# Kernel optimization log

Hardware: AMD Instinct MI355X
Metric: run time of the kernel (lower is better)

Reference implementation:

```python
import jax, jax.numpy as jnp
import numpy as np

DIM = 256
H_GLOBAL = 8
H_LOCAL = 4  # max(1, num_heads // 2)
WINDOW = 5
HALF = WINDOW // 2
B, S = 4, 2048
EPS = 1e-5


def layer_norm(x, g, b):
    mu = jnp.mean(x, axis=-1, keepdims=True)
    var = jnp.mean(jnp.square(x - mu), axis=-1, keepdims=True)
    return (x - mu) * jax.lax.rsqrt(var + EPS) * g + b


def qkv_proj(x, in_w, in_b):
    qkv = x @ in_w.T + in_b
    return jnp.split(qkv, 3, axis=-1)


def global_mha(x, in_w, in_b, out_w, out_b, nh):
    Bq, Sq, D = x.shape
    hd = D // nh
    q, k, v = qkv_proj(x, in_w, in_b)
    q = q.reshape(Bq, Sq, nh, hd)
    k = k.reshape(Bq, Sq, nh, hd)
    v = v.reshape(Bq, Sq, nh, hd)
    scores = jnp.einsum('bqhd,bkhd->bhqk', q, k) / np.sqrt(hd).astype(np.float32)
    attn = jax.nn.softmax(scores, axis=-1)
    o = jnp.einsum('bhqk,bkhd->bqhd', attn, v).reshape(Bq, Sq, D)
    return o @ out_w.T + out_b


def local_mha(x, in_w, in_b, out_w, out_b, nh):
    # banded sliding-window attention, window = 2*HALF+1, per-query softmax
    Bq, Sq, D = x.shape
    hd = D // nh
    q, k, v = qkv_proj(x, in_w, in_b)
    kp = jnp.pad(k, ((0, 0), (HALF, HALF), (0, 0)))
    vp = jnp.pad(v, ((0, 0), (HALF, HALF), (0, 0)))
    # [B, S, W, D] windows of keys/values around each query position
    k_win = jnp.stack([kp[:, j:j + Sq] for j in range(WINDOW)], axis=2)
    v_win = jnp.stack([vp[:, j:j + Sq] for j in range(WINDOW)], axis=2)
    q = q.reshape(Bq, Sq, nh, hd)
    k_win = k_win.reshape(Bq, Sq, WINDOW, nh, hd)
    v_win = v_win.reshape(Bq, Sq, WINDOW, nh, hd)
    scores = jnp.einsum('bshd,bswhd->bshw', q, k_win) / np.sqrt(hd).astype(np.float32)
    idx = jnp.arange(Sq)[:, None] + jnp.arange(-HALF, HALF + 1)[None, :]  # [S, W]
    valid = (idx >= 0) & (idx < Sq)
    scores = jnp.where(valid[None, :, None, :], scores, -jnp.inf)
    attn = jax.nn.softmax(scores, axis=-1)
    o = jnp.einsum('bshw,bswhd->bshd', attn, v_win).reshape(Bq, Sq, D)
    return o @ out_w.T + out_b


def setup_inputs() -> dict:
    key = jax.random.key(0)
    ks = jax.random.split(key, 8)
    sc = 0.02
    d = DIM
    return {
        'x': jax.random.normal(ks[0], (B, S, d), jnp.float32),
        'g_in_w': jax.random.normal(ks[1], (3 * d, d), jnp.float32) * sc,
        'g_in_b': jnp.zeros((3 * d,), jnp.float32),
        'g_out_w': jax.random.normal(ks[2], (d, d), jnp.float32) * sc,
        'g_out_b': jnp.zeros((d,), jnp.float32),
        't_in_w': jax.random.normal(ks[3], (3 * d, d), jnp.float32) * sc,
        't_in_b': jnp.zeros((3 * d,), jnp.float32),
        't_out_w': jax.random.normal(ks[4], (d, d), jnp.float32) * sc,
        't_out_b': jnp.zeros((d,), jnp.float32),
        'fus_w1': jax.random.normal(ks[5], (2 * d, 2 * d), jnp.float32) * sc,
        'fus_b1': jnp.zeros((2 * d,), jnp.float32),
        'fus_w2': jax.random.normal(ks[6], (d, 2 * d), jnp.float32) * sc,
        'fus_b2': jnp.zeros((d,), jnp.float32),
        'ffn_w1': jax.random.normal(ks[7], (2 * d, d), jnp.float32) * sc,
        'ffn_b1': jnp.zeros((2 * d,), jnp.float32),
        'ffn_w2': jax.random.normal(jax.random.fold_in(key, 9), (d, 2 * d), jnp.float32) * sc,
        'ffn_b2': jnp.zeros((d,), jnp.float32),
        'gn_g': jnp.ones((d,), jnp.float32),
        'gn_b': jnp.zeros((d,), jnp.float32),
        'fn_g': jnp.ones((d,), jnp.float32),
        'fn_b': jnp.zeros((d,), jnp.float32),
    }


def reference(x, g_in_w, g_in_b, g_out_w, g_out_b,
              t_in_w, t_in_b, t_out_w, t_out_b,
              fus_w1, fus_b1, fus_w2, fus_b2,
              ffn_w1, ffn_b1, ffn_w2, ffn_b2,
              gn_g, gn_b, fn_g, fn_b):
    x_global = global_mha(x, g_in_w, g_in_b, g_out_w, g_out_b, H_GLOBAL)
    x_local = local_mha(x, t_in_w, t_in_b, t_out_w, t_out_b, H_LOCAL)
    x_comb = jnp.concatenate([x_global, x_local], axis=-1)
    x_fused = jax.nn.silu(x_comb @ fus_w1.T + fus_b1) @ fus_w2.T + fus_b2
    x = layer_norm(x + x_fused, gn_g, gn_b)
    x_ffn = jax.nn.silu(x @ ffn_w1.T + ffn_b1) @ ffn_w2.T + ffn_b2
    x = layer_norm(x + x_ffn, fn_g, fn_b)
    return x
```

## Files before the change

### kernel.cpp

```cpp
#include <hip/hip_runtime.h>

constexpr int Bb = 4;
constexpr int Ss = 2048;
constexpr int QSTR = 1536;

typedef __bf16 bf16x8 __attribute__((ext_vector_type(8)));
typedef __bf16 bf16x4 __attribute__((ext_vector_type(4)));
typedef float  f32x4  __attribute__((ext_vector_type(4)));
typedef unsigned int uint2v __attribute__((ext_vector_type(2)));
typedef unsigned int uint4v __attribute__((ext_vector_type(4)));

__device__ __forceinline__ void glds16(const void* g, void* l) {
    __builtin_amdgcn_global_load_lds(
        (const __attribute__((address_space(1))) unsigned int*)g,
        (__attribute__((address_space(3))) unsigned int*)l, 16, 0, 0);
}

__device__ __forceinline__ void xpose4(unsigned int& a, unsigned int& b) {
    uint2v r = __builtin_amdgcn_permlane32_swap(a, b, false, false);
    uint2v u = __builtin_amdgcn_permlane16_swap(r[0], r[1], false, false);
    a = u[0]; b = u[1];
}

__device__ __forceinline__ unsigned int exp2_pk(float a, float b) {
    float ea = __builtin_amdgcn_exp2f(a);
    float eb = __builtin_amdgcn_exp2f(b);
    unsigned int r;
    asm("v_cvt_pk_bf16_f32 %0, %1, %2" : "=v"(r) : "v"(ea), "v"(eb));
    return r;
}

struct CvtArgs {
    const float* src[9];
    __bf16* dst[9];
    int start[10];
};

__global__ __launch_bounds__(256) void convert_all(CvtArgs a)
{
    int e = 0;
    const int bid = blockIdx.x;
#pragma unroll
    for (int i = 0; i < 8; i++) if (bid >= a.start[i + 1]) e = i + 1;
    const int idx = (bid - a.start[e]) * 256 + threadIdx.x;
    const float* s = a.src[e];
    float4 v0 = *(const float4*)&s[(size_t)idx * 8];
    float4 v1 = *(const float4*)&s[(size_t)idx * 8 + 4];
    bf16x8 o;
    o[0] = (__bf16)v0.x; o[1] = (__bf16)v0.y; o[2] = (__bf16)v0.z; o[3] = (__bf16)v0.w;
    o[4] = (__bf16)v1.x; o[5] = (__bf16)v1.y; o[6] = (__bf16)v1.z; o[7] = (__bf16)v1.w;
    *(bf16x8*)&a.dst[e][(size_t)idx * 8] = o;
}

__global__ __launch_bounds__(256) void gemm128(
    const __bf16* __restrict__ A, const __bf16* __restrict__ W,
    const float* __restrict__ bias, const float* __restrict__ bias2, int bsplit,
    __bf16* __restrict__ C, int K, int ldc)
{
    __shared__ __bf16 As[128 * 64];
    __shared__ __bf16 Ws[128 * 64];
    const int tid = threadIdx.x;
    const int lane = tid & 63;
    const int wv = tid >> 6;
    const int wm = (wv >> 1) * 64;
    const int wn = (wv & 1) * 64;
    const int qrow = lane & 15;
    const int quad = lane >> 4;
    const int n0 = blockIdx.x * 128;
    const int m0 = blockIdx.y * 128;

    f32x4 acc[4][4];
#pragma unroll
    for (int i = 0; i < 4; i++)
#pragma unroll
        for (int j = 0; j < 4; j++) acc[i][j] = {0.f, 0.f, 0.f, 0.f};

    for (int k0 = 0; k0 < K; k0 += 64) {
        __syncthreads();
#pragma unroll
        for (int i = 0; i < 4; i++) {
            const int c = (wv * 4 + i) * 64 + lane;
            const int row = c >> 3, g = c & 7;
            const int gs = (g ^ (row & 7)) * 8;
            glds16(&A[(size_t)(m0 + row) * K + k0 + gs], &As[(wv * 4 + i) * 512]);
            glds16(&W[(size_t)(n0 + row) * K + k0 + gs], &Ws[(wv * 4 + i) * 512]);
        }
        __syncthreads();
#pragma unroll
        for (int ksub = 0; ksub < 2; ksub++) {
            const int gl = ksub * 4 + quad;
            bf16x8 af[4], bf[4];
#pragma unroll
            for (int mi = 0; mi < 4; mi++) {
                const int row = wm + mi * 16 + qrow;
                af[mi] = *(const bf16x8*)&As[row * 64 + (gl ^ (row & 7)) * 8];
            }
#pragma unroll
            for (int ni = 0; ni < 4; ni++) {
                const int row = wn + ni * 16 + qrow;
                bf[ni] = *(const bf16x8*)&Ws[row * 64 + (gl ^ (row & 7)) * 8];
            }
#pragma unroll
            for (int mi = 0; mi < 4; mi++)
#pragma unroll
                for (int ni = 0; ni < 4; ni++)
                    acc[mi][ni] = __builtin_amdgcn_mfma_f32_16x16x32_bf16(
                        af[mi], bf[ni], acc[mi][ni], 0, 0, 0);
        }
    }

    float bz[4];
#pragma unroll
    for (int ni = 0; ni < 4; ni++) {
        const int n = n0 + wn + ni * 16 + qrow;
        bz[ni] = (n < bsplit) ? bias[n] : bias2[n - bsplit];
    }
#pragma unroll
    for (int mi = 0; mi < 4; mi++)
#pragma unroll
        for (int r = 0; r < 4; r++) {
            const int row = m0 + wm + mi * 16 + quad * 4 + r;
#pragma unroll
            for (int ni = 0; ni < 4; ni++) {
                float v = acc[mi][ni][r] + bz[ni];
                C[(size_t)row * ldc + n0 + wn + ni * 16 + qrow] = (__bf16)v;
            }
        }
}

template<bool SILU, bool OUT_BF16>
__global__ __launch_bounds__(256) void gemm_mid(
    const __bf16* __restrict__ A0, const __bf16* __restrict__ W0,
    const float* __restrict__ bias0, const __bf16* __restrict__ W1,
    const float* __restrict__ bias1, int nsplit, int aoff1, int coff1,
    void* __restrict__ C, int lda, int K, int ldc)
{
    __shared__ __bf16 As[64 * 128];
    __shared__ __bf16 Ws[64 * 128];
    const int tid = threadIdx.x;
    const int lane = tid & 63;
    const int wv = tid >> 6;
    const int wm = (wv >> 1) * 32;
    const int wn = (wv & 1) * 32;
    const int qrow = lane & 15;
    const int quad = lane >> 4;
    const bool second = (int)blockIdx.x >= nsplit;
    const int bx = second ? (blockIdx.x - nsplit) : blockIdx.x;
    const __bf16* A = second ? (A0 + aoff1) : A0;
    const __bf16* W = second ? W1 : W0;
    const float* bias = second ? bias1 : bias0;
    const int coff = second ? coff1 : 0;
    const int n0 = bx * 64;
    const int m0 = blockIdx.y * 64;

    f32x4 acc[2][2];
#pragma unroll
    for (int i = 0; i < 2; i++)
#pragma unroll
        for (int j = 0; j < 2; j++) acc[i][j] = {0.f, 0.f, 0.f, 0.f};

    for (int k0 = 0; k0 < K; k0 += 128) {
        __syncthreads();
#pragma unroll
        for (int i = 0; i < 4; i++) {
            const int c = (wv * 4 + i) * 64 + lane;
            const int row = c >> 4, s = c & 15;
            const int gs = ((s & 8) | ((s ^ row) & 7)) * 8;
            glds16(&A[(size_t)(m0 + row) * lda + k0 + gs], &As[(wv * 4 + i) * 512]);
            glds16(&W[(size_t)(n0 + row) * K + k0 + gs], &Ws[(wv * 4 + i) * 512]);
        }
        __syncthreads();
#pragma unroll
        for (int ksub = 0; ksub < 4; ksub++) {
            const int gl = ksub * 4 + quad;
            bf16x8 af[2], bf[2];
#pragma unroll
            for (int mi = 0; mi < 2; mi++) {
                const int row = wm + mi * 16 + qrow;
                const int s = (gl & 8) | ((gl ^ row) & 7);
                af[mi] = *(const bf16x8*)&As[row * 128 + s * 8];
            }
#pragma unroll
            for (int ni = 0; ni < 2; ni++) {
                const int row = wn + ni * 16 + qrow;
                const int s = (gl & 8) | ((gl ^ row) & 7);
                bf[ni] = *(const bf16x8*)&Ws[row * 128 + s * 8];
            }
#pragma unroll
            for (int mi = 0; mi < 2; mi++)
#pragma unroll
                for (int ni = 0; ni < 2; ni++)
                    acc[mi][ni] = __builtin_amdgcn_mfma_f32_16x16x32_bf16(
                        af[mi], bf[ni], acc[mi][ni], 0, 0, 0);
        }
    }

    float bz[2];
#pragma unroll
    for (int ni = 0; ni < 2; ni++) bz[ni] = bias[n0 + wn + ni * 16 + qrow];

#pragma unroll
    for (int mi = 0; mi < 2; mi++)
#pragma unroll
        for (int r = 0; r < 4; r++) {
            const int row = m0 + wm + mi * 16 + quad * 4 + r;
#pragma unroll
            for (int ni = 0; ni < 2; ni++) {
                float v = acc[mi][ni][r] + bz[ni];
                if (SILU) v = v / (1.f + __expf(-v));
                const int col = coff + n0 + wn + ni * 16 + qrow;
                if (OUT_BF16)
                    ((__bf16*)C)[(size_t)row * ldc + col] = (__bf16)v;
                else
                    ((float*)C)[(size_t)row * ldc + col] = v;
            }
        }
}

template<bool OBF>
__global__ __launch_bounds__(256) void gemm_ln(
    const __bf16* __restrict__ A, const __bf16* __restrict__ W,
    const float* __restrict__ bias, const float* __restrict__ res,
    const float* __restrict__ g, const float* __restrict__ be,
    float* __restrict__ out, __bf16* __restrict__ outb)
{
    __shared__ __bf16 As[16 * 128];
    __shared__ __bf16 Ws[256 * 128];
    __shared__ float lnp[2][16][4];
    const int tid = threadIdx.x;
    const int lane = tid & 63;
    const int wv = tid >> 6;
    const int qrow = lane & 15;
    const int quad = lane >> 4;
    const int m0 = blockIdx.x * 16;

    f32x4 acc[4];
#pragma unroll
    for (int ni = 0; ni < 4; ni++) acc[ni] = {0.f, 0.f, 0.f, 0.f};

    for (int k0 = 0; k0 < 512; k0 += 128) {
        __syncthreads();
        {
            const int c = wv * 64 + lane;
            const int row = c >> 4, s = c & 15;
            const int gs = ((s & 8) | ((s ^ row) & 7)) * 8;
            glds16(&A[(size_t)(m0 + row) * 512 + k0 + gs], &As[wv * 512]);
        }
#pragma unroll
        for (int i = 0; i < 16; i++) {
            const int c = (wv * 16 + i) * 64 + lane;
            const int row = c >> 4, s = c & 15;
            const int gs = ((s & 8) | ((s ^ row) & 7)) * 8;
            glds16(&W[(size_t)row * 512 + k0 + gs], &Ws[(wv * 16 + i) * 512]);
        }
        __syncthreads();
#pragma unroll
        for (int ksub = 0; ksub < 4; ksub++) {
            const int gl = ksub * 4 + quad;
            bf16x8 af, bf[4];
            {
                const int row = qrow;
                const int s = (gl & 8) | ((gl ^ row) & 7);
                af = *(const bf16x8*)&As[row * 128 + s * 8];
            }
#pragma unroll
            for (int ni = 0; ni < 4; ni++) {
                const int row = wv * 64 + ni * 16 + qrow;
                const int s = (gl & 8) | ((gl ^ row) & 7);
                bf[ni] = *(const bf16x8*)&Ws[row * 128 + s * 8];
            }
#pragma unroll
            for (int ni = 0; ni < 4; ni++)
                acc[ni] = __builtin_amdgcn_mfma_f32_16x16x32_bf16(
                    af, bf[ni], acc[ni], 0, 0, 0);
        }
    }

    f32x4 d[4];
#pragma unroll
    for (int ni = 0; ni < 4; ni++) {
        const int f = wv * 64 + ni * 16 + qrow;
        const float bz = bias[f];
#pragma unroll
        for (int r = 0; r < 4; r++)
            d[ni][r] = acc[ni][r] + bz + res[(size_t)(m0 + quad * 4 + r) * 256 + f];
    }

    f32x4 ps;
#pragma unroll
    for (int r = 0; r < 4; r++) ps[r] = d[0][r] + d[1][r] + d[2][r] + d[3][r];
#pragma unroll
    for (int off = 1; off <= 8; off <<= 1)
#pragma unroll
        for (int r = 0; r < 4; r++) ps[r] += __shfl_xor(ps[r], off, 64);
    if (qrow == 0)
#pragma unroll
        for (int r = 0; r < 4; r++) lnp[0][quad * 4 + r][wv] = ps[r];
    __syncthreads();
    float mu[4];
#pragma unroll
    for (int r = 0; r < 4; r++) {
        const int t = quad * 4 + r;
        mu[r] = (lnp[0][t][0] + lnp[0][t][1] + lnp[0][t][2] + lnp[0][t][3]) * (1.f / 256.f);
    }

#pragma unroll
    for (int r = 0; r < 4; r++) {
        float a0 = d[0][r] - mu[r], a1 = d[1][r] - mu[r];
        float a2 = d[2][r] - mu[r], a3 = d[3][r] - mu[r];
        ps[r] = a0 * a0 + a1 * a1 + a2 * a2 + a3 * a3;
    }
#pragma unroll
    for (int off = 1; off <= 8; off <<= 1)
#pragma unroll
        for (int r = 0; r < 4; r++) ps[r] += __shfl_xor(ps[r], off, 64);
    if (qrow == 0)
#pragma unroll
        for (int r = 0; r < 4; r++) lnp[1][quad * 4 + r][wv] = ps[r];
    __syncthreads();
    float rsv[4];
#pragma unroll
    for (int r = 0; r < 4; r++) {
        const int t = quad * 4 + r;
        float v = (lnp[1][t][0] + lnp[1][t][1] + lnp[1][t][2] + lnp[1][t][3]) * (1.f / 256.f);
        rsv[r] = rsqrtf(v + 1e-5f);
    }

#pragma unroll
    for (int ni = 0; ni < 4; ni++) {
        const int f = wv * 64 + ni * 16 + qrow;
        const float gg = g[f];
        const float bb = be[f];
#pragma unroll
        for (int r = 0; r < 4; r++) {
            const size_t idx = (size_t)(m0 + quad * 4 + r) * 256 + f;
            float o = (d[ni][r] - mu[r]) * rsv[r] * gg + bb;
            out[idx] = o;
            if (OBF) outb[idx] = (__bf16)o;
        }
    }
}

__global__ __launch_bounds__(512) void attn_fused(
    const __bf16* __restrict__ qkv, __bf16* __restrict__ Op,
    float* __restrict__ Lp, __bf16* __restrict__ acat)
{
    __shared__ __bf16 Kl[2][64 * 32];
    __shared__ __bf16 Vt[2][32 * 72];

    const int t = threadIdx.x;
    const int lane = t & 63;
    const int wv = t >> 6;

    if (blockIdx.x < 1024) {
        const int bid = blockIdx.x;
        const int sp = bid & 3;
        const int qc = (bid >> 2) & 7;
        const int h  = (bid >> 5) & 7;
        const int b  = bid >> 8;
        const int bS = b * Ss;
        const int q0 = qc * 256;

        const int qrow = lane & 15;
        const int quad = lane >> 4;
        const float cQ = 1.4426950408889634f * 0.17677669529663687f;

        bf16x8 qf[2];
#pragma unroll
        for (int tl = 0; tl < 2; tl++) {
            bf16x8 qraw = *(const bf16x8*)(qkv +
                (size_t)(bS + q0 + wv * 32 + tl * 16 + qrow) * QSTR + h * 32 + quad * 8);
#pragma unroll
            for (int i = 0; i < 8; i++) qf[tl][i] = (__bf16)((float)qraw[i] * cQ);
        }
        bf16x8 ones;
#pragma unroll
        for (int i = 0; i < 8; i++) ones[i] = (__bf16)1.0f;

        f32x4 o0[2], o1[2], lac[2];
#pragma unroll
        for (int tl = 0; tl < 2; tl++) {
            o0[tl] = {0.f, 0.f, 0.f, 0.f};
            o1[tl] = {0.f, 0.f, 0.f, 0.f};
            lac[tl] = {0.f, 0.f, 0.f, 0.f};
        }
        const f32x4 z = {0.f, 0.f, 0.f, 0.f};

        const int kc_c = wv * 64 + lane;
        const int kkey = kc_c >> 2, kdg = kc_c & 3;
        const int vkey = t & 63, vq = t >> 6;
        const int kc0 = sp * 8;

        bf16x4 vreg = *(const bf16x4*)(qkv +
            (size_t)(bS + kc0 * 64 + vkey) * QSTR + 512 + h * 32 + vq * 4);
        if (wv < 4)
            glds16(qkv + (size_t)(bS + kc0 * 64 + kkey) * QSTR + 256 + h * 32 + kdg * 8,
                   &Kl[0][wv * 512]);

        for (int i = 0; i < 8; i++) {
            const int cur = i & 1;
#pragma unroll
            for (int e = 0; e < 4; e++) Vt[cur][(vq * 4 + e) * 72 + vkey] = vreg[e];
            __syncthreads();
            const int nx = (i < 7) ? (kc0 + i + 1) : (kc0 + 7);
            vreg = *(const bf16x4*)(qkv +
                (size_t)(bS + nx * 64 + vkey) * QSTR + 512 + h * 32 + vq * 4);
            if (i < 7 && wv < 4)
                glds16(qkv + (size_t)(bS + nx * 64 + kkey) * QSTR + 256 + h * 32 + kdg * 8,
                       &Kl[1 - cur][wv * 512]);

            bf16x8 kf[4];
#pragma unroll
            for (int kg = 0; kg < 4; kg++)
                kf[kg] = *(const bf16x8*)&Kl[cur][(kg * 16 + qrow) * 32 + quad * 8];
            bf16x8 vf00 = *(const bf16x8*)&Vt[cur][qrow * 72 + quad * 8];
            bf16x8 vf01 = *(const bf16x8*)&Vt[cur][qrow * 72 + 32 + quad * 8];
            bf16x8 vf10 = *(const bf16x8*)&Vt[cur][(16 + qrow) * 72 + quad * 8];
            bf16x8 vf11 = *(const bf16x8*)&Vt[cur][(16 + qrow) * 72 + 32 + quad * 8];

#pragma unroll
            for (int tl = 0; tl < 2; tl++) {
                f32x4 s[4];
#pragma unroll
                for (int kg = 0; kg < 4; kg++)
                    s[kg] = __builtin_amdgcn_mfma_f32_16x16x32_bf16(
                        kf[kg], qf[tl], z, 0, 0, 0);
                unsigned int R[4][2];
#pragma unroll
                for (int kg = 0; kg < 4; kg++) {
                    R[kg][0] = exp2_pk(s[kg][0], s[kg][1]);
                    R[kg][1] = exp2_pk(s[kg][2], s[kg][3]);
                }
                xpose4(R[0][0], R[1][0]);
                xpose4(R[0][1], R[1][1]);
                xpose4(R[2][0], R[3][0]);
                xpose4(R[2][1], R[3][1]);
                uint4v p0u = {R[0][0], R[0][1], R[1][0], R[1][1]};
                uint4v p1u = {R[2][0], R[2][1], R[3][0], R[3][1]};
                bf16x8 pf0 = __builtin_bit_cast(bf16x8, p0u);
                bf16x8 pf1 = __builtin_bit_cast(bf16x8, p1u);

                o0[tl] = __builtin_amdgcn_mfma_f32_16x16x32_bf16(vf00, pf0, o0[tl], 0, 0, 0);
                o1[tl] = __builtin_amdgcn_mfma_f32_16x16x32_bf16(vf10, pf0, o1[tl], 0, 0, 0);
                lac[tl] = __builtin_amdgcn_mfma_f32_16x16x32_bf16(ones, pf0, lac[tl], 0, 0, 0);
                o0[tl] = __builtin_amdgcn_mfma_f32_16x16x32_bf16(vf01, pf1, o0[tl], 0, 0, 0);
                o1[tl] = __builtin_amdgcn_mfma_f32_16x16x32_bf16(vf11, pf1, o1[tl], 0, 0, 0);
                lac[tl] = __builtin_amdgcn_mfma_f32_16x16x32_bf16(ones, pf1, lac[tl], 0, 0, 0);
            }
        }

#pragma unroll
        for (int tl = 0; tl < 2; tl++) {
            const int gid = (b * 8 + h) * 2048 + q0 + wv * 32 + tl * 16 + qrow;
            __bf16* po = Op + (size_t)sp * 2097152 + (size_t)gid * 32;
            bf16x4 w0, w1;
#pragma unroll
            for (int r = 0; r < 4; r++) {
                w0[r] = (__bf16)o0[tl][r];
                w1[r] = (__bf16)o1[tl][r];
            }
            *(bf16x4*)&po[quad * 4]      = w0;
            *(bf16x4*)&po[16 + quad * 4] = w1;
            if (quad == 0) Lp[sp * 65536 + gid] = lac[tl][0];
        }
    } else {
        const int w = (blockIdx.x - 1024) * 8 + wv;
        const int g = lane >> 3;
        const int l8 = lane & 7;
        const int R = w * 8 + g;
        const int h = R & 3;
        const int s = (R >> 2) & 2047;
        const int b = R >> 13;

        float qv[8];
        {
            bf16x8 q8 = *(const bf16x8*)&qkv[(size_t)(b * Ss + s) * QSTR + 768 + h * 64 + l8 * 8];
#pragma unroll
            for (int e = 0; e < 8; e++) qv[e] = (float)q8[e];
        }

        float sc[5];
        bf16x8 v8[5];
#pragma unroll
        for (int j = 0; j < 5; j++) {
            int pos = s + j - 2;
            bool valid = (pos >= 0) && (pos < Ss);
            int cpos = valid ? pos : 0;
            const size_t rb = (size_t)(b * Ss + cpos) * QSTR;
            bf16x8 k8 = *(const bf16x8*)&qkv[rb + 1024 + h * 64 + l8 * 8];
            v8[j]     = *(const bf16x8*)&qkv[rb + 1280 + h * 64 + l8 * 8];
            float p = 0.f;
#pragma unroll
            for (int e = 0; e < 8; e++) p += qv[e] * (float)k8[e];
            p += __shfl_xor(p, 1, 64);
            p += __shfl_xor(p, 2, 64);
            p += __shfl_xor(p, 4, 64);
            sc[j] = valid ? p * 0.125f : -1e30f;
        }
        float m = sc[0];
#pragma unroll
        for (int j = 1; j < 5; j++) m = fmaxf(m, sc[j]);
        float l = 0.f;
        float o[8];
#pragma unroll
        for (int e = 0; e < 8; e++) o[e] = 0.f;
#pragma unroll
        for (int j = 0; j < 5; j++) {
            float pe = __builtin_amdgcn_exp2f((sc[j] - m) * 1.4426950408889634f);
            l += pe;
#pragma unroll
            for (int e = 0; e < 8; e++) o[e] += pe * (float)v8[j][e];
        }
        const float li = 1.f / l;
        bf16x8 r;
#pragma unroll
        for (int e = 0; e < 8; e++) r[e] = (__bf16)(o[e] * li);
        *(bf16x8*)&acat[(size_t)(b * Ss + s) * 512 + 256 + h * 64 + l8 * 8] = r;
    }
}

__global__ __launch_bounds__(256) void attn_combine(
    const __bf16* __restrict__ Op, const float* __restrict__ Lp,
    __bf16* __restrict__ acat)
{
    const int t = blockIdx.x * 256 + threadIdx.x;
    const int gid = t >> 3;
    const int dg = t & 7;
    const int b = gid >> 14;
    const int h = (gid >> 11) & 7;
    const int q = gid & 2047;

    const float li = 1.f / (Lp[gid] + Lp[65536 + gid] +
                            Lp[131072 + gid] + Lp[196608 + gid]);
    const __bf16* base = Op + (size_t)gid * 32 + dg * 4;
    bf16x4 a0 = *(const bf16x4*)&base[0];
    bf16x4 a1 = *(const bf16x4*)&base[2097152];
    bf16x4 a2 = *(const bf16x4*)&base[4194304];
    bf16x4 a3 = *(const bf16x4*)&base[6291456];
    bf16x4 r;
#pragma unroll
    for (int i = 0; i < 4; i++)
        r[i] = (__bf16)(((float)a0[i] + (float)a1[i] +
                         (float)a2[i] + (float)a3[i]) * li);
    *(bf16x4*)&acat[(size_t)(b * Ss + q) * 512 + h * 32 + dg * 4] = r;
}

extern "C" void kernel_launch(void* const* d_in, const int* in_sizes, int n_in,
                              void* d_out, int out_size, void* d_ws, size_t ws_size,
                              hipStream_t stream)
{
    const float* x      = (const float*)d_in[0];
    const float* g_in_w = (const float*)d_in[1];
    const float* g_in_b = (const float*)d_in[2];
    const float* g_out_w= (const float*)d_in[3];
    const float* g_out_b= (const float*)d_in[4];
    const float* t_in_w = (const float*)d_in[5];
    const float* t_in_b = (const float*)d_in[6];
    const float* t_out_w= (const float*)d_in[7];
    const float* t_out_b= (const float*)d_in[8];
    const float* fus_w1 = (const float*)d_in[9];
    const float* fus_b1 = (const float*)d_in[10];
    const float* fus_w2 = (const float*)d_in[11];
    const float* fus_b2 = (const float*)d_in[12];
    const float* ffn_w1 = (const float*)d_in[13];
    const float* ffn_b1 = (const float*)d_in[14];
    const float* ffn_w2 = (const float*)d_in[15];
    const float* ffn_b2 = (const float*)d_in[16];
    const float* gn_g   = (const float*)d_in[17];
    const float* gn_b   = (const float*)d_in[18];
    const float* fn_g   = (const float*)d_in[19];
    const float* fn_b   = (const float*)d_in[20];
    float* out = (float*)d_out;
    float* ws  = (float*)d_ws;

    __bf16* xb     = (__bf16*)(ws);
    __bf16* wb     = (__bf16*)(ws + 1048576);
    __bf16* qkvgl  = (__bf16*)(ws + 1638400);
    __bf16* acat   = (__bf16*)(ws + 7929856);
    __bf16* fcomb  = (__bf16*)(ws + 10027008);
    __bf16* h1     = (__bf16*)(ws + 12124160);
    float*  x2     = ws + 16318464;
    __bf16* x2b    = (__bf16*)(ws + 18415616);
    __bf16* h2     = h1;
    __bf16* Op = (__bf16*)(ws + 10027008);
    float*  Lp = ws + 18415616;

    __bf16* w_gin  = wb;
    __bf16* w_gout = wb + 393216;
    __bf16* w_tout = wb + 458752;
    __bf16* w_f1   = wb + 524288;
    __bf16* w_f2   = wb + 786432;
    __bf16* w_n1   = wb + 917504;
    __bf16* w_n2   = wb + 1048576;

    CvtArgs ca;
    ca.src[0] = x;      ca.dst[0] = xb;
    ca.src[1] = g_in_w; ca.dst[1] = w_gin;
    ca.src[2] = t_in_w; ca.dst[2] = w_gin + 196608;
    ca.src[3] = g_out_w;ca.dst[3] = w_gout;
    ca.src[4] = t_out_w;ca.dst[4] = w_tout;
    ca.src[5] = fus_w1; ca.dst[5] = w_f1;
    ca.src[6] = fus_w2; ca.dst[6] = w_f2;
    ca.src[7] = ffn_w1; ca.dst[7] = w_n1;
    ca.src[8] = ffn_w2; ca.dst[8] = w_n2;
    int st[10] = {0, 1024, 1120, 1216, 1248, 1280, 1408, 1472, 1536, 1600};
    for (int i = 0; i < 10; i++) ca.start[i] = st[i];

    convert_all<<<dim3(1600), 256, 0, stream>>>(ca);

    gemm128<<<dim3(12, 64), 256, 0, stream>>>(
        xb, w_gin, g_in_b, t_in_b, 768, qkvgl, 256, QSTR);
    attn_fused<<<dim3(1536), 512, 0, stream>>>(qkvgl, Op, Lp, acat);
    attn_combine<<<dim3(2048), 256, 0, stream>>>(Op, Lp, acat);
    gemm_mid<false, true><<<dim3(8, 128), 256, 0, stream>>>(
        acat, w_gout, g_out_b, w_tout, t_out_b, 4, 256, 256, fcomb, 512, 256, 512);
    gemm_mid<true,  true><<<dim3(8, 128), 256, 0, stream>>>(
        fcomb, w_f1, fus_b1, w_f1, fus_b1, 1 << 30, 0, 0, h1, 512, 512, 512);
    gemm_ln<true><<<dim3(512), 256, 0, stream>>>(
        h1, w_f2, fus_b2, x, gn_g, gn_b, x2, x2b);
    gemm_mid<true,  true><<<dim3(8, 128), 256, 0, stream>>>(
        x2b, w_n1, ffn_b1, w_n1, ffn_b1, 1 << 30, 0, 0, h2, 256, 256, 512);
    gemm_ln<false><<<dim3(512), 256, 0, stream>>>(
        h2, w_n2, ffn_b2, x2, fn_g, fn_b, out, nullptr);
}
```

Measured before the change: 207.2 us.

## Fuse split-K attention combine into output projection GEMM A-tile loading

```diff
diff --git a/kernel.cpp b/kernel.cpp
--- a/kernel.cpp
+++ b/kernel.cpp
@@ -217,6 +217,112 @@
         }
 }
 
+__global__ __launch_bounds__(256) void gemm_out(
+    const __bf16* __restrict__ Op, const float* __restrict__ Lp,
+    const __bf16* __restrict__ acat,
+    const __bf16* __restrict__ w_gout, const float* __restrict__ g_out_b,
+    const __bf16* __restrict__ w_tout, const float* __restrict__ t_out_b,
+    __bf16* __restrict__ C)
+{
+    __shared__ __bf16 As[64 * 128];
+    __shared__ __bf16 Ws[64 * 128];
+    const int tid = threadIdx.x;
+    const int lane = tid & 63;
+    const int wv = tid >> 6;
+    const int wm = (wv >> 1) * 32;
+    const int wn = (wv & 1) * 32;
+    const int qrow = lane & 15;
+    const int quad = lane >> 4;
+    const bool second = (int)blockIdx.x >= 4;
+    const int bx = second ? (blockIdx.x - 4) : blockIdx.x;
+    const __bf16* W = second ? w_tout : w_gout;
+    const float* bias = second ? t_out_b : g_out_b;
+    const int coff = second ? 256 : 0;
+    const int n0 = bx * 64;
+    const int m0 = blockIdx.y * 64;
+
+    f32x4 acc[2][2];
+#pragma unroll
+    for (int i = 0; i < 2; i++)
+#pragma unroll
+        for (int j = 0; j < 2; j++) acc[i][j] = {0.f, 0.f, 0.f, 0.f};
+
+    for (int k0 = 0; k0 < 256; k0 += 128) {
+        __syncthreads();
+#pragma unroll
+        for (int i = 0; i < 4; i++) {
+            const int c = (wv * 4 + i) * 64 + lane;
+            const int row = c >> 4, s = c & 15;
+            const int gs = ((s & 8) | ((s ^ row) & 7)) * 8;
+            if (second) {
+                glds16(&acat[(size_t)(m0 + row) * 512 + 256 + k0 + gs],
+                       &As[(wv * 4 + i) * 512]);
+            } else {
+                const int k = k0 + gs;
+                const int tok = m0 + row;
+                const int bq = tok >> 11, q = tok & 2047;
+                const int h = k >> 5, d = k & 31;
+                const size_t gid = (size_t)(bq * 8 + h) * 2048 + q;
+                const float li = 1.f / (Lp[gid] + Lp[65536 + gid] +
+                                        Lp[131072 + gid] + Lp[196608 + gid]);
+                const __bf16* base = Op + gid * 32 + d;
+                bf16x8 a0 = *(const bf16x8*)&base[0];
+                bf16x8 a1 = *(const bf16x8*)&base[2097152];
+                bf16x8 a2 = *(const bf16x8*)&base[4194304];
+                bf16x8 a3 = *(const bf16x8*)&base[6291456];
+                bf16x8 o;
+#pragma unroll
+                for (int p = 0; p < 8; p++)
+                    o[p] = (__bf16)(((float)a0[p] + (float)a1[p] +
+                                     (float)a2[p] + (float)a3[p]) * li);
+                *(bf16x8*)&As[(size_t)c * 8] = o;
+            }
+            glds16(&W[(size_t)(n0 + row) * 256 + k0 + gs], &Ws[(wv * 4 + i) * 512]);
+        }
+        __syncthreads();
+#pragma unroll
+        for (int ksub = 0; ksub < 4; ksub++) {
+            const int gl = ksub * 4 + quad;
+            bf16x8 af[2], bf[2];
+#pragma unroll
+            for (int mi = 0; mi < 2; mi++) {
+                const int row = wm + mi * 16 + qrow;
+                const int s = (gl & 8) | ((gl ^ row) & 7);
+                af[mi] = *(const bf16x8*)&As[row * 128 + s * 8];
+            }
+#pragma unroll
+            for (int ni = 0; ni < 2; ni++) {
+                const int row = wn + ni * 16 + qrow;
+                const int s = (gl & 8) | ((gl ^ row) & 7);
+                bf[ni] = *(const bf16x8*)&Ws[row * 128 + s * 8];
+            }
+#pragma unroll
+            for (int mi = 0; mi < 2; mi++)
+#pragma unroll
+                for (int ni = 0; ni < 2; ni++)
+                    acc[mi][ni] = __builtin_amdgcn_mfma_f32_16x16x32_bf16(
+                        af[mi], bf[ni], acc[mi][ni], 0, 0, 0);
+        }
+    }
+
+    float bz[2];
+#pragma unroll
+    for (int ni = 0; ni < 2; ni++) bz[ni] = bias[n0 + wn + ni * 16 + qrow];
+
+#pragma unroll
+    for (int mi = 0; mi < 2; mi++)
+#pragma unroll
+        for (int r = 0; r < 4; r++) {
+            const int row = m0 + wm + mi * 16 + quad * 4 + r;
+#pragma unroll
+            for (int ni = 0; ni < 2; ni++) {
+                float v = acc[mi][ni][r] + bz[ni];
+                const int col = coff + n0 + wn + ni * 16 + qrow;
+                C[(size_t)row * 512 + col] = (__bf16)v;
+            }
+        }
+}
+
 template<bool OBF>
 __global__ __launch_bounds__(256) void gemm_ln(
     const __bf16* __restrict__ A, const __bf16* __restrict__ W,
@@ -517,32 +623,6 @@
         for (int e = 0; e < 8; e++) r[e] = (__bf16)(o[e] * li);
         *(bf16x8*)&acat[(size_t)(b * Ss + s) * 512 + 256 + h * 64 + l8 * 8] = r;
     }
-}
-
-__global__ __launch_bounds__(256) void attn_combine(
-    const __bf16* __restrict__ Op, const float* __restrict__ Lp,
-    __bf16* __restrict__ acat)
-{
-    const int t = blockIdx.x * 256 + threadIdx.x;
-    const int gid = t >> 3;
-    const int dg = t & 7;
-    const int b = gid >> 14;
-    const int h = (gid >> 11) & 7;
-    const int q = gid & 2047;
-
-    const float li = 1.f / (Lp[gid] + Lp[65536 + gid] +
-                            Lp[131072 + gid] + Lp[196608 + gid]);
-    const __bf16* base = Op + (size_t)gid * 32 + dg * 4;
-    bf16x4 a0 = *(const bf16x4*)&base[0];
-    bf16x4 a1 = *(const bf16x4*)&base[2097152];
-    bf16x4 a2 = *(const bf16x4*)&base[4194304];
-    bf16x4 a3 = *(const bf16x4*)&base[6291456];
-    bf16x4 r;
-#pragma unroll
-    for (int i = 0; i < 4; i++)
-        r[i] = (__bf16)(((float)a0[i] + (float)a1[i] +
-                         (float)a2[i] + (float)a3[i]) * li);
-    *(bf16x4*)&acat[(size_t)(b * Ss + q) * 512 + h * 32 + dg * 4] = r;
 }
 
 extern "C" void kernel_launch(void* const* d_in, const int* in_sizes, int n_in,
@@ -579,11 +659,11 @@
     __bf16* acat   = (__bf16*)(ws + 7929856);
     __bf16* fcomb  = (__bf16*)(ws + 10027008);
     __bf16* h1     = (__bf16*)(ws + 12124160);
+    __bf16* Op = (__bf16*)(ws + 14221312);
     float*  x2     = ws + 16318464;
+    float*  Lp = ws + 18415616;
     __bf16* x2b    = (__bf16*)(ws + 18415616);
     __bf16* h2     = h1;
-    __bf16* Op = (__bf16*)(ws + 10027008);
-    float*  Lp = ws + 18415616;
 
     __bf16* w_gin  = wb;
     __bf16* w_gout = wb + 393216;
@@ -611,9 +691,8 @@
     gemm128<<<dim3(12, 64), 256, 0, stream>>>(
         xb, w_gin, g_in_b, t_in_b, 768, qkvgl, 256, QSTR);
     attn_fused<<<dim3(1536), 512, 0, stream>>>(qkvgl, Op, Lp, acat);
-    attn_combine<<<dim3(2048), 256, 0, stream>>>(Op, Lp, acat);
-    gemm_mid<false, true><<<dim3(8, 128), 256, 0, stream>>>(
-        acat, w_gout, g_out_b, w_tout, t_out_b, 4, 256, 256, fcomb, 512, 256, 512);
+    gemm_out<<<dim3(8, 128), 256, 0, stream>>>(
+        Op, Lp, acat, w_gout, g_out_b, w_tout, t_out_b, fcomb);
     gemm_mid<true,  true><<<dim3(8, 128), 256, 0, stream>>>(
         fcomb, w_f1, fus_b1, w_f1, fus_b1, 1 << 30, 0, 0, h1, 512, 512, 512);
     gemm_ln<true><<<dim3(512), 256, 0, stream>>>(
```

Result: slower. 213.4 us (+3.0%).
